# Kernel optimization log

Measured on AMD Instinct MI355X. Metric: run time of the kernel, lower is better.

The kernel has to match this reference:

```python
import jax, jax.numpy as jnp
from jax import lax
import numpy as np

B, T = 4096, 32
VOCAB, E, H, NCLS = 10000, 300, 300, 2


def setup_inputs() -> dict:
    key = jax.random.key(0)
    ks = jax.random.split(key, 10)
    cap = jax.random.randint(ks[0], (B, T), 0, VOCAB)
    cap_len = jax.random.randint(ks[1], (B,), 1, T + 1)  # lengths in [1, T]
    embed_w = jax.random.uniform(ks[2], (VOCAB, E), jnp.float32, -0.1, 0.1)
    s = 1.0 / np.sqrt(H)
    W_ih = jax.random.uniform(ks[3], (4 * H, E), jnp.float32, -s, s)
    W_hh = jax.random.uniform(ks[4], (4 * H, H), jnp.float32, -s, s)
    b_ih = jax.random.uniform(ks[5], (4 * H,), jnp.float32, -s, s)
    b_hh = jax.random.uniform(ks[6], (4 * H,), jnp.float32, -s, s)
    cls_v = jax.random.normal(ks[7], (NCLS, H), jnp.float32) * 0.05
    cls_g = jnp.linalg.norm(cls_v, axis=1, keepdims=True)  # weight_norm init: g = ||v||
    cls_b = jax.random.uniform(ks[8], (NCLS,), jnp.float32, -s, s)
    return {"cap": cap, "cap_len": cap_len, "embed_w": embed_w,
            "W_ih": W_ih, "W_hh": W_hh, "b_ih": b_ih, "b_hh": b_hh,
            "cls_v": cls_v, "cls_g": cls_g, "cls_b": cls_b}


def _lstm_forward(cap, cap_len, embed_w, W_ih, W_hh, b_ih, b_hh, cls_v, cls_g, cls_b):
    bsz = cap.shape[0]
    hid = W_hh.shape[1]
    emb = embed_w[cap]                                   # [B, T, E]
    # Precompute the input projections for all timesteps at once (one big GEMM).
    x_gates = jnp.einsum('bte,ge->btg', emb, W_ih) + b_ih + b_hh  # [B, T, 4H]

    def step(carry, xg_t):
        h, c = carry
        gates = xg_t + h @ W_hh.T                        # [B, 4H]
        i, f, g, o = jnp.split(gates, 4, axis=-1)        # torch gate order i,f,g,o
        i = jax.nn.sigmoid(i)
        f = jax.nn.sigmoid(f)
        g = jnp.tanh(g)
        o = jax.nn.sigmoid(o)
        c = f * c + i * g
        h = o * jnp.tanh(c)
        return (h, c), h

    h0 = jnp.zeros((bsz, hid), emb.dtype)
    (_, _), hs = lax.scan(step, (h0, h0), jnp.swapaxes(x_gates, 0, 1))  # hs: [T, B, H]
    h_last = hs[cap_len - 1, jnp.arange(bsz)]            # last valid hidden state per sample
    # weight-normed classifier: W = g * v / ||v||_row  (dropout is identity in eval)
    W = cls_g * cls_v / jnp.linalg.norm(cls_v, axis=1, keepdims=True)
    return h_last @ W.T + cls_b


def reference(cap, cap_len, embed_w, W_ih, W_hh, b_ih, b_hh, cls_v, cls_g, cls_b):
    return _lstm_forward(cap, cap_len, embed_w, W_ih, W_hh, b_ih, b_hh, cls_v, cls_g, cls_b)
```

## Files before the change

### kernel.cpp

```cpp
#include <hip/hip_runtime.h>
#include <hip/hip_fp16.h>

typedef _Float16 f16;
typedef _Float16 f16x4 __attribute__((ext_vector_type(4)));
typedef _Float16 f16x8 __attribute__((ext_vector_type(8)));
typedef float f32x4 __attribute__((ext_vector_type(4)));

#define B_SZ   4096
#define T_SZ   32
#define VOCAB  10000
#define E_SZ   300
#define H_SZ   300
#define KP     320
#define GP     304
#define G4     1216
#define LDA    328
#define LDG    1224
#define LDX    1224
#define LDC    308
#define ROWS   16
#define NBLK   (B_SZ/ROWS)

__device__ __forceinline__ float sigmoid_f(float x) {
    return 1.f / (1.f + __expf(-x));
}
__device__ __forceinline__ float tanh_f(float x) {
    return 2.f / (1.f + __expf(-2.f * x)) - 1.f;
}

__global__ void kP0(const float* __restrict__ ew, f16* __restrict__ embT) {
    int v = blockIdx.x, k = threadIdx.x;
    embT[(size_t)v * KP + k] = (k < E_SZ) ? (f16)ew[(size_t)v * E_SZ + k] : (f16)0.f;
}

__global__ void kPW2(const float* __restrict__ wih, const float* __restrict__ whh,
                     const float* __restrict__ bih, const float* __restrict__ bhh,
                     f16* __restrict__ Wpk, float* __restrict__ biasp) {
    int bid = blockIdx.x;
    int lane = threadIdx.x;
    int k = bid % 20, ntg = bid / 20;
    int nt = ntg % 19, gate = ntg / 19;
    int c = lane & 15, q = lane >> 4;
    int j = nt * 16 + c;
    int src = gate * H_SZ + j;
    f16 vals[8];
#pragma unroll
    for (int jj = 0; jj < 8; ++jj) {
        int kk = k * 32 + q * 8 + jj;
        float v = 0.f;
        if (j < H_SZ) {
            if (kk < KP) { if (kk < H_SZ) v = whh[(size_t)src * H_SZ + kk]; }
            else { int kx = kk - KP; if (kx < E_SZ) v = wih[(size_t)src * E_SZ + kx]; }
        }
        vals[jj] = (f16)v;
    }
    *(f16x8*)(Wpk + ((size_t)bid * 64 + lane) * 8) = *(const f16x8*)vals;
    if (k == 0 && q == 0)
        biasp[gate * GP + j] = (j < H_SZ) ? (bih[src] + bhh[src]) : 0.f;
}

__global__ void kPW4(const float* __restrict__ whh, f16* __restrict__ WgS) {
    int bid = blockIdx.x;
    int lane = threadIdx.x;
    int c = lane & 15, q = lane >> 4;
    f16 vals[8];
    if (bid < 760) {
        int nt = bid / 40, g = (bid % 40) / 10, k = bid % 10;
        int j = nt * 16 + c;
        int src = g * H_SZ + j;
#pragma unroll
        for (int jj = 0; jj < 8; ++jj) {
            int kk = k * 32 + q * 8 + jj;
            float v = (j < H_SZ && kk < H_SZ) ? whh[(size_t)src * H_SZ + kk] : 0.f;
            vals[jj] = (f16)v;
        }
    } else {
#pragma unroll
        for (int jj = 0; jj < 8; ++jj) vals[jj] = (f16)0.f;
    }
    *(f16x8*)(WgS + ((size_t)bid * 64 + lane) * 8) = *(const f16x8*)vals;
}

__global__ void kP2(const float* __restrict__ cls_v, const float* __restrict__ cls_g,
                    float* __restrict__ Wc) {
    int lane = threadIdx.x;
    for (int cl = 0; cl < 2; ++cl) {
        float s = 0.f;
        for (int j = lane; j < H_SZ; j += 64) { float v = cls_v[cl * H_SZ + j]; s += v * v; }
        for (int off = 32; off; off >>= 1) s += __shfl_down(s, off);
        float nrm = sqrtf(__shfl(s, 0));
        float scale = cls_g[cl] / nrm;
        for (int j = lane; j < H_SZ; j += 64) Wc[cl * GP + j] = cls_v[cl * H_SZ + j] * scale;
    }
}

__global__ __launch_bounds__(512, 2)
void kX2(const f16* __restrict__ embT, const f16* __restrict__ Wpk,
         const float* __restrict__ biasp, f16* __restrict__ embX) {
    int tid = threadIdx.x;
    int v0 = blockIdx.x * 16;
    int wave = tid >> 6, lane = tid & 63;
    int c = lane & 15, q = lane >> 4;
    int gate = wave >> 1, half = wave & 1;
    int nt0 = half * 10, ntiles = half ? 9 : 10;
    const f16* wp0 = Wpk + (((size_t)(gate * 19 + nt0) * 20 + 10) * 64 + lane) * 8;
    f16x8 afr[10];
    const f16* arow = embT + (size_t)(v0 + c) * KP + q * 8;
#pragma unroll
    for (int k = 0; k < 10; ++k)
        afr[k] = *(const f16x8*)(arow + k * 32);
    f16x8 buf[10];
#pragma unroll
    for (int s = 0; s < 10; ++s)
        buf[s] = *(const f16x8*)(wp0 + (size_t)s * 512);
#pragma unroll 1
    for (int nt = 0; nt < ntiles - 1; ++nt) {
        int jcol = (nt0 + nt) * 16 + c;
        float bia = biasp[gate * GP + jcol];
        f32x4 acc = {bia, bia, bia, bia};
#pragma unroll
        for (int k = 0; k < 10; ++k) {
            acc = __builtin_amdgcn_mfma_f32_16x16x32_f16(afr[k], buf[k], acc, 0, 0, 0);
            buf[k] = *(const f16x8*)(wp0 + (size_t)(nt * 20 + k + 20) * 512);
        }
#pragma unroll
        for (int r = 0; r < 4; ++r)
            embX[((size_t)(v0 + q * 4 + r) * GP + jcol) * 4 + gate] = (f16)acc[r];
    }
    {
        int nt = ntiles - 1;
        int jcol = (nt0 + nt) * 16 + c;
        float bia = biasp[gate * GP + jcol];
        f32x4 acc = {bia, bia, bia, bia};
#pragma unroll
        for (int k = 0; k < 10; ++k)
            acc = __builtin_amdgcn_mfma_f32_16x16x32_f16(afr[k], buf[k], acc, 0, 0, 0);
#pragma unroll
        for (int r = 0; r < 4; ++r)
            embX[((size_t)(v0 + q * 4 + r) * GP + jcol) * 4 + gate] = (f16)acc[r];
    }
}

__global__ __launch_bounds__(512, 2)
void kR13(const int* __restrict__ cap,
          const int* __restrict__ cap_len,
          const f16* __restrict__ embX,
          const f16* __restrict__ WgS,
          float* __restrict__ hlast) {
    extern __shared__ __align__(16) char smem[];
    f16*   hbufA = (f16*)smem;
    f16*   xst   = (f16*)(smem + 20992);
    float* cbuf  = (float*)(smem + 99328);
    int*   capv  = (int*)(smem + 119040);
    int*   lens  = (int*)(smem + 121088);
    int tid = threadIdx.x;
    int b0 = blockIdx.x * ROWS;
    if (tid < ROWS) lens[tid] = cap_len[b0 + tid];
    for (int i = tid; i < ROWS * T_SZ; i += 512) capv[i] = cap[(size_t)b0 * T_SZ + i];
    for (int i = tid; i < 2 * ROWS * LDA; i += 512) hbufA[i] = (f16)0.f;
    for (int i = tid; i < ROWS * LDC; i += 512) cbuf[i] = 0.f;
    __syncthreads();
    for (int i = tid; i < ROWS * 152; i += 512) {
        int m = i / 152, c8 = i - m * 152;
        int v = capv[m * T_SZ + 0];
        *(f16x8*)(xst + m * LDX + c8 * 8) = *(const f16x8*)(embX + (size_t)v * G4 + c8 * 8);
    }
    __syncthreads();
    int wave = tid >> 6, lane = tid & 63;
    int c = lane & 15, q = lane >> 4;
    int tstart = (wave < 5) ? 2 * wave : 10 + 3 * (wave - 5);
    int tcnt   = (wave < 5) ? 2 : 3;
    const f16* wp0 = WgS + ((size_t)(tstart * 40) * 64 + lane) * 8;
    int tstop[4];
#pragma unroll
    for (int r = 0; r < 4; ++r) tstop[r] = lens[q * 4 + r] - 1;
    int cur = 0;

    for (int t = 0; t < T_SZ; ++t) {
        const f16* hb = hbufA + cur * (ROWS * LDA);
        f16*       hn = hbufA + (cur ^ 1) * (ROWS * LDA);
        const f16* xc = xst + (t & 1) * (ROWS * LDX);
        f16*       xn = xst + ((t + 1) & 1) * (ROWS * LDX);
        int tp1 = t + 1;
        if (tp1 < T_SZ) {
            for (int i = tid; i < ROWS * 152; i += 512) {
                int m = i / 152, c8 = i - m * 152;
                int v = capv[m * T_SZ + tp1];
                *(f16x8*)(xn + m * LDX + c8 * 8) =
                    *(const f16x8*)(embX + (size_t)v * G4 + c8 * 8);
            }
        }
        f16x8 afr[10];
#pragma unroll
        for (int k = 0; k < 10; ++k)
            afr[k] = *(const f16x8*)(hb + c * LDA + k * 32 + q * 8);
        f16x8 buf[10];
#pragma unroll
        for (int s = 0; s < 10; ++s)
            buf[s] = *(const f16x8*)(wp0 + (size_t)s * 512);
#pragma unroll 1
        for (int nt = 0; nt < tcnt; ++nt) {
            int col = (tstart + nt) * 16 + c;
            const f16* wnext = wp0 + (size_t)(nt * 40) * 512;
            f32x4 acc0 = {0.f, 0.f, 0.f, 0.f};
            f32x4 acc1 = {0.f, 0.f, 0.f, 0.f};
            f32x4 acc2 = {0.f, 0.f, 0.f, 0.f};
            f32x4 acc3 = {0.f, 0.f, 0.f, 0.f};
#pragma unroll
            for (int k = 0; k < 10; ++k) {
                acc0 = __builtin_amdgcn_mfma_f32_16x16x32_f16(afr[k], buf[k], acc0, 0, 0, 0);
                buf[k] = *(const f16x8*)(wnext + (size_t)(10 + k) * 512);
            }
#pragma unroll
            for (int k = 0; k < 10; ++k) {
                acc1 = __builtin_amdgcn_mfma_f32_16x16x32_f16(afr[k], buf[k], acc1, 0, 0, 0);
                buf[k] = *(const f16x8*)(wnext + (size_t)(20 + k) * 512);
            }
#pragma unroll
            for (int k = 0; k < 10; ++k) {
                acc2 = __builtin_amdgcn_mfma_f32_16x16x32_f16(afr[k], buf[k], acc2, 0, 0, 0);
                buf[k] = *(const f16x8*)(wnext + (size_t)(30 + k) * 512);
            }
#pragma unroll
            for (int k = 0; k < 10; ++k) {
                acc3 = __builtin_amdgcn_mfma_f32_16x16x32_f16(afr[k], buf[k], acc3, 0, 0, 0);
                buf[k] = *(const f16x8*)(wnext + (size_t)(40 + k) * 512);
            }
#pragma unroll
            for (int r = 0; r < 4; ++r) {
                int row = q * 4 + r;
                f16x4 xi = *(const f16x4*)(xc + row * LDX + col * 4);
                float gi = acc0[r] + (float)xi[0];
                float gf = acc1[r] + (float)xi[1];
                float gg = acc2[r] + (float)xi[2];
                float go = acc3[r] + (float)xi[3];
                float ii = sigmoid_f(gi);
                float ff = sigmoid_f(gf);
                float gt = tanh_f(gg);
                float oo = sigmoid_f(go);
                int ci = row * LDC + col;
                float cn = ff * cbuf[ci] + ii * gt;
                cbuf[ci] = cn;
                float hh = oo * tanh_f(cn);
                hn[row * LDA + col] = (f16)hh;
                if (t == tstop[r]) hlast[(size_t)(b0 + row) * GP + col] = hh;
            }
        }
        __syncthreads();
        cur ^= 1;
    }
}

__global__ __launch_bounds__(512, 2)
void kR8(const int* __restrict__ cap,
         const int* __restrict__ cap_len,
         const f16* __restrict__ embT,
         const f16* __restrict__ Wpk,
         const float* __restrict__ biasp,
         float* __restrict__ hlast) {
    extern __shared__ __align__(16) char smem[];
    f16*   hbuf  = (f16*)smem;
    f16*   xbuf  = (f16*)(smem + 10496);
    f16*   gates = (f16*)(smem + 20992);
    float* biasL = (float*)(smem + 60160);
    int*   capv  = (int*)(smem + 65024);
    int*   lens  = (int*)(smem + 67072);
    int tid = threadIdx.x;
    int b0 = blockIdx.x * 16;
    if (tid < 16) lens[tid] = cap_len[b0 + tid];
    for (int i = tid; i < 16 * T_SZ; i += 512) capv[i] = cap[(size_t)b0 * T_SZ + i];
    for (int i = tid; i < 16 * LDA; i += 512) hbuf[i] = (f16)0.f;
    for (int i = tid; i < G4; i += 512) biasL[i] = biasp[i];
    __syncthreads();
    for (int i = tid; i < 16 * 40; i += 512) {
        int m = i / 40, c8 = i - m * 40;
        int v = capv[m * T_SZ + 0];
        *(f16x8*)(xbuf + m * LDA + c8 * 8) = *(const f16x8*)(embT + (size_t)v * KP + c8 * 8);
    }
    __syncthreads();
    int wave = tid >> 6, lane = tid & 63;
    int c = lane & 15, q = lane >> 4;
    int gate = wave >> 1, half = wave & 1;
    int nt0 = half * 10, ntiles = half ? 9 : 10;
    const f16* wp0 = Wpk + ((size_t)((gate * 19 + nt0) * 20) * 64 + lane) * 8;
    const f16* hrow = hbuf + c * LDA + q * 8;
    const f16* xrow = xbuf + c * LDA + q * 8;
    float creg[10];
#pragma unroll
    for (int i = 0; i < 10; ++i) creg[i] = 0.f;

    for (int t = 0; t < T_SZ; ++t) {
        f16x8 afr[10];
#pragma unroll
        for (int k = 0; k < 10; ++k)
            afr[k] = *(const f16x8*)(hrow + k * 32);
        f16x8 buf[10];
#pragma unroll
        for (int s = 0; s < 10; ++s)
            buf[s] = *(const f16x8*)(wp0 + (size_t)s * 512);
#pragma unroll 1
        for (int nt = 0; nt < ntiles - 1; ++nt) {
            int base = nt * 20;
            int ncol = gate * GP + (nt0 + nt) * 16 + c;
            float bia = biasL[ncol];
            f32x4 acch = {bia, bia, bia, bia};
            f32x4 accx = {0.f, 0.f, 0.f, 0.f};
#pragma unroll
            for (int k = 0; k < 20; ++k) {
                if (k < 10) {
                    acch = __builtin_amdgcn_mfma_f32_16x16x32_f16(afr[k], buf[k % 10], acch, 0, 0, 0);
                } else {
                    f16x8 a = *(const f16x8*)(xrow + (k - 10) * 32);
                    accx = __builtin_amdgcn_mfma_f32_16x16x32_f16(a, buf[k % 10], accx, 0, 0, 0);
                }
                buf[k % 10] = *(const f16x8*)(wp0 + (size_t)(base + k + 10) * 512);
            }
#pragma unroll
            for (int r = 0; r < 4; ++r)
                gates[(q * 4 + r) * LDG + ncol] = (f16)(acch[r] + accx[r]);
        }
        {
            int nt = ntiles - 1;
            int base = nt * 20;
            int ncol = gate * GP + (nt0 + nt) * 16 + c;
            float bia = biasL[ncol];
            f32x4 acch = {bia, bia, bia, bia};
            f32x4 accx = {0.f, 0.f, 0.f, 0.f};
#pragma unroll
            for (int k = 0; k < 20; ++k) {
                if (k < 10) {
                    acch = __builtin_amdgcn_mfma_f32_16x16x32_f16(afr[k], buf[k % 10], acch, 0, 0, 0);
                    buf[k % 10] = *(const f16x8*)(wp0 + (size_t)(base + k + 10) * 512);
                } else {
                    f16x8 a = *(const f16x8*)(xrow + (k - 10) * 32);
                    accx = __builtin_amdgcn_mfma_f32_16x16x32_f16(a, buf[k % 10], accx, 0, 0, 0);
                }
            }
#pragma unroll
            for (int r = 0; r < 4; ++r)
                gates[(q * 4 + r) * LDG + ncol] = (f16)(acch[r] + accx[r]);
        }
        __syncthreads();
        int tp1 = t + 1;
        if (tp1 < T_SZ) {
            for (int i = tid; i < 16 * 40; i += 512) {
                int m = i / 40, c8 = i - m * 40;
                int v = capv[m * T_SZ + tp1];
                *(f16x8*)(xbuf + m * LDA + c8 * 8) =
                    *(const f16x8*)(embT + (size_t)v * KP + c8 * 8);
            }
        }
#pragma unroll
        for (int it = 0; it < 10; ++it) {
            int idx = tid + it * 512;
            int m = idx / 320, j = idx - m * 320;
            if (j < H_SZ) {
                const f16* gr = gates + m * LDG;
                float gi = (float)gr[j];
                float gf = (float)gr[GP + j];
                float gg = (float)gr[2 * GP + j];
                float go = (float)gr[3 * GP + j];
                float ii = sigmoid_f(gi);
                float ff = sigmoid_f(gf);
                float gt = tanh_f(gg);
                float oo = sigmoid_f(go);
                float cn = ff * creg[it] + ii * gt;
                creg[it] = cn;
                float hh = oo * tanh_f(cn);
                hbuf[m * LDA + j] = (f16)hh;
                if (t == lens[m] - 1) hlast[(size_t)(b0 + m) * GP + j] = hh;
            }
        }
        __syncthreads();
    }
}

__global__ void kC(const float* __restrict__ hlast, const float* __restrict__ Wc,
                   const float* __restrict__ cls_b, float* __restrict__ out) {
    int row = blockIdx.x, lane = threadIdx.x;
    const float* h = hlast + (size_t)row * GP;
    float s0 = 0.f, s1 = 0.f;
    for (int j = lane; j < H_SZ; j += 64) {
        float hv = h[j];
        s0 += hv * Wc[j];
        s1 += hv * Wc[GP + j];
    }
    for (int off = 32; off; off >>= 1) {
        s0 += __shfl_down(s0, off);
        s1 += __shfl_down(s1, off);
    }
    if (lane == 0) {
        out[row * 2 + 0] = s0 + cls_b[0];
        out[row * 2 + 1] = s1 + cls_b[1];
    }
}

extern "C" void kernel_launch(void* const* d_in, const int* in_sizes, int n_in,
                              void* d_out, int out_size, void* d_ws, size_t ws_size,
                              hipStream_t stream) {
    const int*   cap     = (const int*)d_in[0];
    const int*   cap_len = (const int*)d_in[1];
    const float* embed_w = (const float*)d_in[2];
    const float* W_ih    = (const float*)d_in[3];
    const float* W_hh    = (const float*)d_in[4];
    const float* b_ih    = (const float*)d_in[5];
    const float* b_hh    = (const float*)d_in[6];
    const float* cls_v   = (const float*)d_in[7];
    const float* cls_g   = (const float*)d_in[8];
    const float* cls_b   = (const float*)d_in[9];
    float* out = (float*)d_out;

    char* w = (char*)d_ws;
    size_t off = 0;
    auto alloc = [&](size_t bytes) -> void* {
        void* p = w + off;
        off += (bytes + 255) & ~(size_t)255;
        return p;
    };
    f16*   embT  = (f16*)alloc((size_t)VOCAB * KP * sizeof(f16));
    f16*   Wpk   = (f16*)alloc((size_t)1520 * 64 * 8 * sizeof(f16));
    f16*   WgS   = (f16*)alloc((size_t)800 * 64 * 8 * sizeof(f16));
    float* biasp = (float*)alloc((size_t)G4 * sizeof(float));
    float* Wc    = (float*)alloc((size_t)2 * GP * sizeof(float));
    float* hlast = (float*)alloc((size_t)B_SZ * GP * sizeof(float));
    f16*   embX  = (f16*)(w + off);
    size_t need_split = off + ((size_t)VOCAB * GP * 4 * sizeof(f16) + 255);
    bool split = (ws_size >= need_split);

    kP0<<<VOCAB, KP, 0, stream>>>(embed_w, embT);
    kPW2<<<1520, 64, 0, stream>>>(W_ih, W_hh, b_ih, b_hh, Wpk, biasp);
    kP2<<<1, 64, 0, stream>>>(cls_v, cls_g, Wc);
    if (split) {
        kPW4<<<800, 64, 0, stream>>>(W_hh, WgS);
        kX2<<<VOCAB / 16, 512, 0, stream>>>(embT, Wpk, biasp, embX);
        static const int smem_r13 = 121152;
        (void)hipFuncSetAttribute((const void*)kR13,
                                  hipFuncAttributeMaxDynamicSharedMemorySize, smem_r13);
        kR13<<<NBLK, 512, smem_r13, stream>>>(cap, cap_len, embX, WgS, hlast);
    } else {
        static const int smem_r8 = 67072 + 64;
        (void)hipFuncSetAttribute((const void*)kR8,
                                  hipFuncAttributeMaxDynamicSharedMemorySize, smem_r8);
        kR8<<<B_SZ / 16, 512, smem_r8, stream>>>(cap, cap_len, embT, Wpk, biasp, hlast);
    }
    kC<<<B_SZ, 64, 0, stream>>>(hlast, Wc, cls_b, out);
}
```

Measured before the change: 422.0 us.

## Process 32 rows per block, keep cell state in registers, read gate inputs directly

The recurrent kernel now handles 32 batch rows per block instead of 16, so each W_hh fragment streamed from global memory feeds two MFMAs, halving weight traffic per row. The cell state moves from shared memory into registers, and the per-step staging of precomputed input gates into shared memory is replaced by direct gathered global loads into registers. The first weight fragments are prefetched once before the time loop and rolled over across timesteps. This roughly doubles register pressure (two A-fragment sets, cell registers), which may limit occupancy. It also halves the grid to 128 blocks, fewer than the CU count, and adds global-load latency inside each timestep.

```diff
diff --git a/kernel.cpp b/kernel.cpp
--- a/kernel.cpp
+++ b/kernel.cpp
@@ -16,10 +16,8 @@
 #define G4     1216
 #define LDA    328
 #define LDG    1224
-#define LDX    1224
-#define LDC    308
-#define ROWS   16
-#define NBLK   (B_SZ/ROWS)
+#define R14    32
+#define NB14   (B_SZ/R14)
 
 __device__ __forceinline__ float sigmoid_f(float x) {
     return 1.f / (1.f + __expf(-x));
@@ -142,108 +140,108 @@
 }
 
 __global__ __launch_bounds__(512, 2)
-void kR13(const int* __restrict__ cap,
+void kR14(const int* __restrict__ cap,
           const int* __restrict__ cap_len,
           const f16* __restrict__ embX,
           const f16* __restrict__ WgS,
           float* __restrict__ hlast) {
-    extern __shared__ __align__(16) char smem[];
-    f16*   hbufA = (f16*)smem;
-    f16*   xst   = (f16*)(smem + 20992);
-    float* cbuf  = (float*)(smem + 99328);
-    int*   capv  = (int*)(smem + 119040);
-    int*   lens  = (int*)(smem + 121088);
+    __shared__ __align__(16) f16 hbufA[2 * R14 * LDA];
+    __shared__ int capv[R14 * T_SZ];
+    __shared__ int lens[R14];
     int tid = threadIdx.x;
-    int b0 = blockIdx.x * ROWS;
-    if (tid < ROWS) lens[tid] = cap_len[b0 + tid];
-    for (int i = tid; i < ROWS * T_SZ; i += 512) capv[i] = cap[(size_t)b0 * T_SZ + i];
-    for (int i = tid; i < 2 * ROWS * LDA; i += 512) hbufA[i] = (f16)0.f;
-    for (int i = tid; i < ROWS * LDC; i += 512) cbuf[i] = 0.f;
+    int b0 = blockIdx.x * R14;
+    if (tid < R14) lens[tid] = cap_len[b0 + tid];
+    for (int i = tid; i < R14 * T_SZ; i += 512) capv[i] = cap[(size_t)b0 * T_SZ + i];
+    for (int i = tid; i < 2 * R14 * LDA; i += 512) hbufA[i] = (f16)0.f;
     __syncthreads();
-    for (int i = tid; i < ROWS * 152; i += 512) {
-        int m = i / 152, c8 = i - m * 152;
-        int v = capv[m * T_SZ + 0];
-        *(f16x8*)(xst + m * LDX + c8 * 8) = *(const f16x8*)(embX + (size_t)v * G4 + c8 * 8);
-    }
-    __syncthreads();
+
     int wave = tid >> 6, lane = tid & 63;
     int c = lane & 15, q = lane >> 4;
     int tstart = (wave < 5) ? 2 * wave : 10 + 3 * (wave - 5);
     int tcnt   = (wave < 5) ? 2 : 3;
     const f16* wp0 = WgS + ((size_t)(tstart * 40) * 64 + lane) * 8;
-    int tstop[4];
-#pragma unroll
-    for (int r = 0; r < 4; ++r) tstop[r] = lens[q * 4 + r] - 1;
+    int tstop[2][4];
+#pragma unroll
+    for (int rt = 0; rt < 2; ++rt)
+#pragma unroll
+        for (int r = 0; r < 4; ++r) tstop[rt][r] = lens[rt * 16 + q * 4 + r] - 1;
+    float creg[3][2][4];
+#pragma unroll
+    for (int nt = 0; nt < 3; ++nt)
+#pragma unroll
+        for (int rt = 0; rt < 2; ++rt)
+#pragma unroll
+            for (int r = 0; r < 4; ++r) creg[nt][rt][r] = 0.f;
     int cur = 0;
 
+    f16x8 buf[10];
+#pragma unroll
+    for (int s = 0; s < 10; ++s)
+        buf[s] = *(const f16x8*)(wp0 + (size_t)s * 512);
+
     for (int t = 0; t < T_SZ; ++t) {
-        const f16* hb = hbufA + cur * (ROWS * LDA);
-        f16*       hn = hbufA + (cur ^ 1) * (ROWS * LDA);
-        const f16* xc = xst + (t & 1) * (ROWS * LDX);
-        f16*       xn = xst + ((t + 1) & 1) * (ROWS * LDX);
-        int tp1 = t + 1;
-        if (tp1 < T_SZ) {
-            for (int i = tid; i < ROWS * 152; i += 512) {
-                int m = i / 152, c8 = i - m * 152;
-                int v = capv[m * T_SZ + tp1];
-                *(f16x8*)(xn + m * LDX + c8 * 8) =
-                    *(const f16x8*)(embX + (size_t)v * G4 + c8 * 8);
-            }
-        }
-        f16x8 afr[10];
-#pragma unroll
-        for (int k = 0; k < 10; ++k)
-            afr[k] = *(const f16x8*)(hb + c * LDA + k * 32 + q * 8);
-        f16x8 buf[10];
-#pragma unroll
-        for (int s = 0; s < 10; ++s)
-            buf[s] = *(const f16x8*)(wp0 + (size_t)s * 512);
-#pragma unroll 1
-        for (int nt = 0; nt < tcnt; ++nt) {
-            int col = (tstart + nt) * 16 + c;
-            const f16* wnext = wp0 + (size_t)(nt * 40) * 512;
-            f32x4 acc0 = {0.f, 0.f, 0.f, 0.f};
-            f32x4 acc1 = {0.f, 0.f, 0.f, 0.f};
-            f32x4 acc2 = {0.f, 0.f, 0.f, 0.f};
-            f32x4 acc3 = {0.f, 0.f, 0.f, 0.f};
-#pragma unroll
-            for (int k = 0; k < 10; ++k) {
-                acc0 = __builtin_amdgcn_mfma_f32_16x16x32_f16(afr[k], buf[k], acc0, 0, 0, 0);
-                buf[k] = *(const f16x8*)(wnext + (size_t)(10 + k) * 512);
-            }
-#pragma unroll
-            for (int k = 0; k < 10; ++k) {
-                acc1 = __builtin_amdgcn_mfma_f32_16x16x32_f16(afr[k], buf[k], acc1, 0, 0, 0);
-                buf[k] = *(const f16x8*)(wnext + (size_t)(20 + k) * 512);
-            }
-#pragma unroll
-            for (int k = 0; k < 10; ++k) {
-                acc2 = __builtin_amdgcn_mfma_f32_16x16x32_f16(afr[k], buf[k], acc2, 0, 0, 0);
-                buf[k] = *(const f16x8*)(wnext + (size_t)(30 + k) * 512);
-            }
-#pragma unroll
-            for (int k = 0; k < 10; ++k) {
-                acc3 = __builtin_amdgcn_mfma_f32_16x16x32_f16(afr[k], buf[k], acc3, 0, 0, 0);
-                buf[k] = *(const f16x8*)(wnext + (size_t)(40 + k) * 512);
-            }
-#pragma unroll
-            for (int r = 0; r < 4; ++r) {
-                int row = q * 4 + r;
-                f16x4 xi = *(const f16x4*)(xc + row * LDX + col * 4);
-                float gi = acc0[r] + (float)xi[0];
-                float gf = acc1[r] + (float)xi[1];
-                float gg = acc2[r] + (float)xi[2];
-                float go = acc3[r] + (float)xi[3];
-                float ii = sigmoid_f(gi);
-                float ff = sigmoid_f(gf);
-                float gt = tanh_f(gg);
-                float oo = sigmoid_f(go);
-                int ci = row * LDC + col;
-                float cn = ff * cbuf[ci] + ii * gt;
-                cbuf[ci] = cn;
-                float hh = oo * tanh_f(cn);
-                hn[row * LDA + col] = (f16)hh;
-                if (t == tstop[r]) hlast[(size_t)(b0 + row) * GP + col] = hh;
+        const f16* hb = hbufA + cur * (R14 * LDA);
+        f16*       hn = hbufA + (cur ^ 1) * (R14 * LDA);
+        int vr[2][4];
+#pragma unroll
+        for (int rt = 0; rt < 2; ++rt)
+#pragma unroll
+            for (int r = 0; r < 4; ++r)
+                vr[rt][r] = capv[(rt * 16 + q * 4 + r) * T_SZ + t];
+        f16x8 afr0[10], afr1[10];
+#pragma unroll
+        for (int k = 0; k < 10; ++k) {
+            afr0[k] = *(const f16x8*)(hb + c * LDA + k * 32 + q * 8);
+            afr1[k] = *(const f16x8*)(hb + (16 + c) * LDA + k * 32 + q * 8);
+        }
+#pragma unroll
+        for (int nt = 0; nt < 3; ++nt) {
+            if (nt < tcnt) {
+                int col = (tstart + nt) * 16 + c;
+                f16x4 xi0[4], xi1[4];
+#pragma unroll
+                for (int r = 0; r < 4; ++r) {
+                    xi0[r] = *(const f16x4*)(embX + (size_t)vr[0][r] * G4 + col * 4);
+                    xi1[r] = *(const f16x4*)(embX + (size_t)vr[1][r] * G4 + col * 4);
+                }
+                f32x4 ac[4][2];
+#pragma unroll
+                for (int g = 0; g < 4; ++g) {
+                    ac[g][0] = (f32x4){0.f, 0.f, 0.f, 0.f};
+                    ac[g][1] = (f32x4){0.f, 0.f, 0.f, 0.f};
+                }
+#pragma unroll
+                for (int g = 0; g < 4; ++g) {
+                    int nb = (g < 3) ? (nt * 40 + (g + 1) * 10)
+                                     : ((nt + 1 < tcnt) ? (nt + 1) * 40 : 0);
+#pragma unroll
+                    for (int k = 0; k < 10; ++k) {
+                        ac[g][0] = __builtin_amdgcn_mfma_f32_16x16x32_f16(afr0[k], buf[k], ac[g][0], 0, 0, 0);
+                        ac[g][1] = __builtin_amdgcn_mfma_f32_16x16x32_f16(afr1[k], buf[k], ac[g][1], 0, 0, 0);
+                        buf[k] = *(const f16x8*)(wp0 + (size_t)(nb + k) * 512);
+                    }
+                }
+#pragma unroll
+                for (int rt = 0; rt < 2; ++rt)
+#pragma unroll
+                    for (int r = 0; r < 4; ++r) {
+                        f16x4 xv = rt ? xi1[r] : xi0[r];
+                        float gi = ac[0][rt][r] + (float)xv[0];
+                        float gf = ac[1][rt][r] + (float)xv[1];
+                        float gg = ac[2][rt][r] + (float)xv[2];
+                        float go = ac[3][rt][r] + (float)xv[3];
+                        float ii = sigmoid_f(gi);
+                        float ff = sigmoid_f(gf);
+                        float gt = tanh_f(gg);
+                        float oo = sigmoid_f(go);
+                        float cn = ff * creg[nt][rt][r] + ii * gt;
+                        creg[nt][rt][r] = cn;
+                        float hh = oo * tanh_f(cn);
+                        int row = rt * 16 + q * 4 + r;
+                        hn[row * LDA + col] = (f16)hh;
+                        if (t == tstop[rt][r])
+                            hlast[(size_t)(b0 + row) * GP + col] = hh;
+                    }
             }
         }
         __syncthreads();
@@ -433,10 +431,7 @@
     if (split) {
         kPW4<<<800, 64, 0, stream>>>(W_hh, WgS);
         kX2<<<VOCAB / 16, 512, 0, stream>>>(embT, Wpk, biasp, embX);
-        static const int smem_r13 = 121152;
-        (void)hipFuncSetAttribute((const void*)kR13,
-                                  hipFuncAttributeMaxDynamicSharedMemorySize, smem_r13);
-        kR13<<<NBLK, 512, smem_r13, stream>>>(cap, cap_len, embX, WgS, hlast);
+        kR14<<<NB14, 512, 0, stream>>>(cap, cap_len, embX, WgS, hlast);
     } else {
         static const int smem_r8 = 67072 + 64;
         (void)hipFuncSetAttribute((const void*)kR8,
```

After: 1.469 ms. +248.1%, slower.

## Keep part of recurrent weights in LDS, gather gate inputs directly, fuse classifier

Applied to the files above, without the earlier changes.

The recurrent kernel now loads a per-wave slice of the W_hh weight tiles into shared memory once and reads them from LDS, instead of streaming every tile from global memory each timestep. It drops the double-buffered shared staging of precomputed input gates and gathers them straight from global memory per tile. The classifier dot product is fused in via shuffle reductions and atomic adds into a zeroed output, removing the separate classifier kernel and the hlast round trip. The trade-offs are a larger shared-memory footprint, global gather latency inside each step, and atomic accumulation.

```diff
diff --git a/kernel.cpp b/kernel.cpp
--- a/kernel.cpp
+++ b/kernel.cpp
@@ -16,7 +16,6 @@
 #define G4     1216
 #define LDA    328
 #define LDG    1224
-#define LDX    1224
 #define LDC    308
 #define ROWS   16
 #define NBLK   (B_SZ/ROWS)
@@ -90,7 +89,8 @@
         for (int off = 32; off; off >>= 1) s += __shfl_down(s, off);
         float nrm = sqrtf(__shfl(s, 0));
         float scale = cls_g[cl] / nrm;
-        for (int j = lane; j < H_SZ; j += 64) Wc[cl * GP + j] = cls_v[cl * H_SZ + j] * scale;
+        for (int j = lane; j < GP; j += 64)
+            Wc[cl * GP + j] = (j < H_SZ) ? cls_v[cl * H_SZ + j] * scale : 0.f;
     }
 }
 
@@ -142,98 +142,94 @@
 }
 
 __global__ __launch_bounds__(512, 2)
-void kR13(const int* __restrict__ cap,
+void kR22(const int* __restrict__ cap,
           const int* __restrict__ cap_len,
           const f16* __restrict__ embX,
           const f16* __restrict__ WgS,
-          float* __restrict__ hlast) {
+          const float* __restrict__ Wc,
+          const float* __restrict__ cls_b,
+          float* __restrict__ out) {
     extern __shared__ __align__(16) char smem[];
     f16*   hbufA = (f16*)smem;
-    f16*   xst   = (f16*)(smem + 20992);
-    float* cbuf  = (float*)(smem + 99328);
-    int*   capv  = (int*)(smem + 119040);
-    int*   lens  = (int*)(smem + 121088);
+    float* cbuf  = (float*)(smem + 20992);
+    int*   capv  = (int*)(smem + 40704);
+    int*   lens  = (int*)(smem + 42752);
+    f16*   wres  = (f16*)(smem + 43008);
     int tid = threadIdx.x;
     int b0 = blockIdx.x * ROWS;
     if (tid < ROWS) lens[tid] = cap_len[b0 + tid];
     for (int i = tid; i < ROWS * T_SZ; i += 512) capv[i] = cap[(size_t)b0 * T_SZ + i];
     for (int i = tid; i < 2 * ROWS * LDA; i += 512) hbufA[i] = (f16)0.f;
     for (int i = tid; i < ROWS * LDC; i += 512) cbuf[i] = 0.f;
-    __syncthreads();
-    for (int i = tid; i < ROWS * 152; i += 512) {
-        int m = i / 152, c8 = i - m * 152;
-        int v = capv[m * T_SZ + 0];
-        *(f16x8*)(xst + m * LDX + c8 * 8) = *(const f16x8*)(embX + (size_t)v * G4 + c8 * 8);
-    }
-    __syncthreads();
+
     int wave = tid >> 6, lane = tid & 63;
     int c = lane & 15, q = lane >> 4;
     int tstart = (wave < 5) ? 2 * wave : 10 + 3 * (wave - 5);
     int tcnt   = (wave < 5) ? 2 : 3;
+    int Rw     = (wave < 5) ? 1 : 2;
+    f16* resw = wres + ((wave < 5) ? wave * 5120 : 25600 + (wave - 5) * 10240);
+    for (int u = 0; u < Rw; ++u)
+#pragma unroll
+        for (int k = 0; k < 10; ++k)
+            *(f16x8*)(resw + (u * 10 + k) * 512 + lane * 8) =
+                *(const f16x8*)(WgS + ((size_t)(tstart * 40 + u * 10 + k) * 64 + lane) * 8);
+    __syncthreads();
+
     const f16* wp0 = WgS + ((size_t)(tstart * 40) * 64 + lane) * 8;
-    int tstop[4];
-#pragma unroll
-    for (int r = 0; r < 4; ++r) tstop[r] = lens[q * 4 + r] - 1;
     int cur = 0;
+    f16x8 buf[10];
+#pragma unroll
+    for (int s = 0; s < 10; ++s)
+        buf[s] = *(const f16x8*)(wp0 + (size_t)(Rw * 10 + s) * 512);
 
     for (int t = 0; t < T_SZ; ++t) {
         const f16* hb = hbufA + cur * (ROWS * LDA);
         f16*       hn = hbufA + (cur ^ 1) * (ROWS * LDA);
-        const f16* xc = xst + (t & 1) * (ROWS * LDX);
-        f16*       xn = xst + ((t + 1) & 1) * (ROWS * LDX);
-        int tp1 = t + 1;
-        if (tp1 < T_SZ) {
-            for (int i = tid; i < ROWS * 152; i += 512) {
-                int m = i / 152, c8 = i - m * 152;
-                int v = capv[m * T_SZ + tp1];
-                *(f16x8*)(xn + m * LDX + c8 * 8) =
-                    *(const f16x8*)(embX + (size_t)v * G4 + c8 * 8);
-            }
-        }
         f16x8 afr[10];
 #pragma unroll
         for (int k = 0; k < 10; ++k)
             afr[k] = *(const f16x8*)(hb + c * LDA + k * 32 + q * 8);
-        f16x8 buf[10];
-#pragma unroll
-        for (int s = 0; s < 10; ++s)
-            buf[s] = *(const f16x8*)(wp0 + (size_t)s * 512);
 #pragma unroll 1
         for (int nt = 0; nt < tcnt; ++nt) {
             int col = (tstart + nt) * 16 + c;
-            const f16* wnext = wp0 + (size_t)(nt * 40) * 512;
+            f16x4 xi[4];
+#pragma unroll
+            for (int r = 0; r < 4; ++r) {
+                int v = capv[(q * 4 + r) * T_SZ + t];
+                xi[r] = *(const f16x4*)(embX + (size_t)v * G4 + col * 4);
+            }
             f32x4 acc0 = {0.f, 0.f, 0.f, 0.f};
             f32x4 acc1 = {0.f, 0.f, 0.f, 0.f};
             f32x4 acc2 = {0.f, 0.f, 0.f, 0.f};
             f32x4 acc3 = {0.f, 0.f, 0.f, 0.f};
 #pragma unroll
-            for (int k = 0; k < 10; ++k) {
-                acc0 = __builtin_amdgcn_mfma_f32_16x16x32_f16(afr[k], buf[k], acc0, 0, 0, 0);
-                buf[k] = *(const f16x8*)(wnext + (size_t)(10 + k) * 512);
-            }
-#pragma unroll
-            for (int k = 0; k < 10; ++k) {
-                acc1 = __builtin_amdgcn_mfma_f32_16x16x32_f16(afr[k], buf[k], acc1, 0, 0, 0);
-                buf[k] = *(const f16x8*)(wnext + (size_t)(20 + k) * 512);
-            }
-#pragma unroll
-            for (int k = 0; k < 10; ++k) {
-                acc2 = __builtin_amdgcn_mfma_f32_16x16x32_f16(afr[k], buf[k], acc2, 0, 0, 0);
-                buf[k] = *(const f16x8*)(wnext + (size_t)(30 + k) * 512);
-            }
-#pragma unroll
-            for (int k = 0; k < 10; ++k) {
-                acc3 = __builtin_amdgcn_mfma_f32_16x16x32_f16(afr[k], buf[k], acc3, 0, 0, 0);
-                buf[k] = *(const f16x8*)(wnext + (size_t)(40 + k) * 512);
+            for (int g = 0; g < 4; ++g) {
+                f32x4* ag = (g == 0) ? &acc0 : (g == 1) ? &acc1 : (g == 2) ? &acc2 : &acc3;
+                if (nt == 0 && g < Rw) {
+                    const f16* rb = resw + g * 5120 + lane * 8;
+#pragma unroll
+                    for (int k = 0; k < 10; ++k)
+                        *ag = __builtin_amdgcn_mfma_f32_16x16x32_f16(
+                            afr[k], *(const f16x8*)(rb + k * 512), *ag, 0, 0, 0);
+                } else {
+                    int nbase = (g < 3) ? (nt * 40 + (g + 1) * 10)
+                              : ((nt + 1 < tcnt) ? (nt + 1) * 40 : Rw * 10);
+#pragma unroll
+                    for (int k = 0; k < 10; ++k) {
+                        *ag = __builtin_amdgcn_mfma_f32_16x16x32_f16(
+                            afr[k], buf[k], *ag, 0, 0, 0);
+                        buf[k] = *(const f16x8*)(wp0 + (size_t)(nbase + k) * 512);
+                    }
+                }
             }
 #pragma unroll
             for (int r = 0; r < 4; ++r) {
                 int row = q * 4 + r;
-                f16x4 xi = *(const f16x4*)(xc + row * LDX + col * 4);
-                float gi = acc0[r] + (float)xi[0];
-                float gf = acc1[r] + (float)xi[1];
-                float gg = acc2[r] + (float)xi[2];
-                float go = acc3[r] + (float)xi[3];
+                f16x4 xv = xi[r];
+                float gi = acc0[r] + (float)xv[0];
+                float gf = acc1[r] + (float)xv[1];
+                float gg = acc2[r] + (float)xv[2];
+                float go = acc3[r] + (float)xv[3];
                 float ii = sigmoid_f(gi);
                 float ff = sigmoid_f(gf);
                 float gt = tanh_f(gg);
@@ -243,7 +239,19 @@
                 cbuf[ci] = cn;
                 float hh = oo * tanh_f(cn);
                 hn[row * LDA + col] = (f16)hh;
-                if (t == tstop[r]) hlast[(size_t)(b0 + row) * GP + col] = hh;
+                if (t == lens[row] - 1) {
+                    float s0 = hh * Wc[col];
+                    float s1 = hh * Wc[GP + col];
+                    s0 += __shfl_xor(s0, 1); s1 += __shfl_xor(s1, 1);
+                    s0 += __shfl_xor(s0, 2); s1 += __shfl_xor(s1, 2);
+                    s0 += __shfl_xor(s0, 4); s1 += __shfl_xor(s1, 4);
+                    s0 += __shfl_xor(s0, 8); s1 += __shfl_xor(s1, 8);
+                    if (c == 0) {
+                        if (wave == 0 && nt == 0) { s0 += cls_b[0]; s1 += cls_b[1]; }
+                        atomicAdd(out + (size_t)(b0 + row) * 2 + 0, s0);
+                        atomicAdd(out + (size_t)(b0 + row) * 2 + 1, s1);
+                    }
+                }
             }
         }
         __syncthreads();
@@ -431,17 +439,18 @@
     kPW2<<<1520, 64, 0, stream>>>(W_ih, W_hh, b_ih, b_hh, Wpk, biasp);
     kP2<<<1, 64, 0, stream>>>(cls_v, cls_g, Wc);
     if (split) {
+        (void)hipMemsetAsync(out, 0, (size_t)out_size, stream);
         kPW4<<<800, 64, 0, stream>>>(W_hh, WgS);
         kX2<<<VOCAB / 16, 512, 0, stream>>>(embT, Wpk, biasp, embX);
-        static const int smem_r13 = 121152;
-        (void)hipFuncSetAttribute((const void*)kR13,
-                                  hipFuncAttributeMaxDynamicSharedMemorySize, smem_r13);
-        kR13<<<NBLK, 512, smem_r13, stream>>>(cap, cap_len, embX, WgS, hlast);
+        static const int smem_r22 = 155648;
+        (void)hipFuncSetAttribute((const void*)kR22,
+                                  hipFuncAttributeMaxDynamicSharedMemorySize, smem_r22);
+        kR22<<<NBLK, 512, smem_r22, stream>>>(cap, cap_len, embX, WgS, Wc, cls_b, out);
     } else {
         static const int smem_r8 = 67072 + 64;
         (void)hipFuncSetAttribute((const void*)kR8,
                                   hipFuncAttributeMaxDynamicSharedMemorySize, smem_r8);
         kR8<<<B_SZ / 16, 512, smem_r8, stream>>>(cap, cap_len, embT, Wpk, biasp, hlast);
-    }
-    kC<<<B_SZ, 64, 0, stream>>>(hlast, Wc, cls_b, out);
-}
+        kC<<<B_SZ, 64, 0, stream>>>(hlast, Wc, cls_b, out);
+    }
+}
```

Measured after the change: 409.4 us. 3.0% less time.
